# Kernel optimization log

Measured on AMD Instinct MI355X. Metric: run time of the kernel, lower is better.

Reference implementation:

```python
import jax, jax.numpy as jnp
import numpy as np

SIZES = (20, 20, 20, 20, 20)          # formula_oh_sizes
OH_N = sum(SIZES)                      # 100
NUM_BINS = 65536                       # spect_bin.get_num_bins()
EPS_SIZE = 1e-4                        # eps added to subset size
IN_EPS = 1e-5                          # torch InstanceNorm1d default eps


def thermometer_oh(counts):
    # StructuredOneHot with accum=True: per-element thermometer encoding.
    # counts: (N, E) element counts -> (N, sum(SIZES)) with out[j]=1 iff j < count.
    outs = [(jnp.arange(s, dtype=counts.dtype)[None, :] < counts[:, i:i + 1]).astype(jnp.float32)
            for i, s in enumerate(SIZES)]
    return jnp.concatenate(outs, axis=-1)


def inorm(x):
    # InstanceNorm1d (affine=False) as applied here: normalize over last dim per row.
    m = jnp.mean(x, axis=-1, keepdims=True)
    v = jnp.var(x, axis=-1, keepdims=True)
    return (x - m) * jax.lax.rsqrt(v + IN_EPS)


def _lin(key, fan_in, fan_out):
    k1, k2 = jax.random.split(key)
    bound = 1.0 / np.sqrt(fan_in)
    W = jax.random.uniform(k1, (fan_in, fan_out), jnp.float32, -bound, bound)
    b = jax.random.uniform(k2, (fan_out,), jnp.float32, -bound, bound)
    return W, b


def setup_inputs():
    key = jax.random.key(0)
    ks = jax.random.split(key, 12)
    B, A, GF, S, P, E, D = 8, 48, 256, 4096, 32, 5, 256
    vert_feat_in = jax.random.normal(ks[0], (B, A, GF), jnp.float32)
    vert_mask_in = jnp.ones((B, A), jnp.float32)
    elem_idx = jax.random.randint(ks[1], (B, A), 0, E)
    vert_element_oh = jax.nn.one_hot(elem_idx, E, dtype=jnp.float32)
    adj_oh = jnp.zeros((B, A, A), jnp.float32)                      # unused by forward path
    atom_subsets = jax.random.randint(ks[2], (B, S, A), 0, 2).astype(jnp.int32)
    atom_subsets_peaks = jnp.zeros((1,), jnp.float32)               # unused (mass_idx/intensity used)
    mass_idx = jax.random.randint(ks[3], (B, S, P), 0, NUM_BINS).astype(jnp.int32)
    intensity = jax.random.uniform(ks[4], (B, S, P), jnp.float32)
    combine_W, combine_b = _lin(ks[5], OH_N + GF, GF)
    l1_W, l1_b = _lin(ks[6], GF, D)
    l2a_W, l2a_b = _lin(ks[7], D, D)
    l2b_W, l2b_b = _lin(ks[8], D, D)
    score_W, score_b = _lin(ks[9], D, 1)
    return {
        'vert_feat_in': vert_feat_in, 'vert_mask_in': vert_mask_in,
        'vert_element_oh': vert_element_oh, 'adj_oh': adj_oh,
        'atom_subsets': atom_subsets, 'atom_subsets_peaks': atom_subsets_peaks,
        'mass_idx': mass_idx, 'intensity': intensity,
        'combine_W': combine_W, 'combine_b': combine_b,
        'l1_W': l1_W, 'l1_b': l1_b, 'l2a_W': l2a_W, 'l2a_b': l2a_b,
        'l2b_W': l2b_W, 'l2b_b': l2b_b, 'score_W': score_W, 'score_b': score_b,
    }


def reference(vert_feat_in, vert_mask_in, vert_element_oh, adj_oh, atom_subsets,
              atom_subsets_peaks, mass_idx, intensity,
              combine_W, combine_b, l1_W, l1_b, l2a_W, l2a_b, l2b_W, l2b_b,
              score_W, score_b):
    B, A, GF = vert_feat_in.shape
    _, S, _ = atom_subsets.shape
    subsets_f = atom_subsets.astype(jnp.float32)
    masked_vert = vert_feat_in * vert_mask_in[:, :, None]               # (B,A,GF)
    subsets_masked = subsets_f * vert_mask_in[:, None, :]               # (B,S,A)
    # weighted sum of vertex features over each subset
    sws = jnp.einsum('bag,bsa->bsg', masked_vert, subsets_masked)        # (B,S,GF)
    # per-subset element counts -> structured one-hot formula encoding
    counts = jnp.einsum('bae,bsa->bse', vert_element_oh, subsets_f)      # (B,S,E)
    pf_oh = thermometer_oh(counts.reshape(-1, counts.shape[-1])).reshape(B, S, OH_N)
    subset_size = jnp.sum(subsets_masked, axis=2) + EPS_SIZE             # (B,S)
    mean_feat = sws / subset_size[:, :, None]
    normed = inorm(mean_feat)                                            # subset_weighted_norm
    combined = jax.nn.relu(jnp.concatenate([pf_oh, normed], -1) @ combine_W + combine_b)
    x = inorm(combined)                                                  # norm_post_combine
    x = jax.nn.relu(x @ l1_W + l1_b)
    x = jax.nn.leaky_relu(x @ l2a_W + l2a_b)
    x = jax.nn.leaky_relu(x @ l2b_W + l2b_b)
    x = jax.nn.relu(x)
    x = inorm(x)                                                         # norm_pre_score
    scores = (x @ score_W + score_b)[..., 0]                             # (B,S)
    probs = jax.nn.softmax(scores, axis=-1)
    # per-batch sparse mass-matrix binning: scatter-add intensity*prob into spectral bins
    weighted = intensity * probs[:, :, None]                             # (B,S,P)
    seg = jax.vmap(lambda idx, w: jax.ops.segment_sum(w, idx, num_segments=NUM_BINS))
    spect_out = seg(mass_idx.reshape(B, -1), weighted.reshape(B, -1))    # (B,NUM_BINS)
    return spect_out, probs
```

## Files before the change

### kernel.cpp

```cpp
#include <hip/hip_runtime.h>
#include <math.h>

#define B_DIM 8
#define A_DIM 48
#define GF_DIM 256
#define S_DIM 4096
#define P_DIM 32
#define E_DIM 5
#define OHN 100
#define NBINS 65536

typedef __attribute__((ext_vector_type(8))) short short8v;
typedef __attribute__((ext_vector_type(4))) float float4v;

__device__ __forceinline__ float wave_sum(float v) {
#pragma unroll
    for (int o = 32; o; o >>= 1) v += __shfl_xor(v, o, 64);
    return v;
}
__device__ __forceinline__ float wave_max(float v) {
#pragma unroll
    for (int o = 32; o; o >>= 1) v = fmaxf(v, __shfl_xor(v, o, 64));
    return v;
}
__device__ __forceinline__ float quad16_sum(float v) {
    v += __shfl_xor(v, 1, 64); v += __shfl_xor(v, 2, 64);
    v += __shfl_xor(v, 4, 64); v += __shfl_xor(v, 8, 64);
    return v;
}
__device__ __forceinline__ unsigned short bf16_rn(float x) {
    unsigned int u = __float_as_uint(x);
    return (unsigned short)((u + 0x7FFFu + ((u >> 16) & 1u)) >> 16);
}
__device__ __forceinline__ float bf16_val(unsigned short h) {
    return __uint_as_float(((unsigned int)h) << 16);
}
__device__ __forceinline__ float therm_val(int j, float c0, float c1, float c2,
                                           float c3, float c4) {
    int e = j / 20;
    int pos = j - e * 20;
    float ce = (e == 0) ? c0 : (e == 1) ? c1 : (e == 2) ? c2 : (e == 3) ? c3 : c4;
    return ((float)pos < ce) ? 1.0f : 0.0f;
}
__device__ __forceinline__ void g2l16(float* lds, const float* g) {
    __builtin_amdgcn_global_load_lds(
        (const __attribute__((address_space(1))) void*)g,
        (__attribute__((address_space(3))) void*)lds,
        16, 0, 0);
}

__global__ __launch_bounds__(256) void k_wprep(
    const float* __restrict__ cW, const float* __restrict__ l1W,
    const float* __restrict__ l2aW, const float* __restrict__ l2bW,
    short* __restrict__ wp)
{
    int e = blockIdx.x * 256 + threadIdx.x;
    int c = e >> 13;
    int i = e & 8191;
    int nt = i >> 9, lane = (i >> 3) & 63, j = i & 7;
    int krel = (lane >> 4) * 8 + j;
    int n = nt * 16 + (lane & 15);
    float val = 0.f;
    if (c < 12) {
        int kp = c * 32 + krel;
        if (kp < 100)       val = cW[kp * 256 + n];
        else if (kp >= 128) val = cW[(kp - 28) * 256 + n];
    } else {
        int L = (c - 12) >> 3;
        int kc = (c - 12) & 7;
        const float* W = (L == 0) ? l1W : (L == 1) ? l2aW : l2bW;
        val = W[(kc * 32 + krel) * 256 + n];
    }
    unsigned short h = bf16_rn(val);
    float lo = val - bf16_val(h);
    wp[c * 16384 + i]        = (short)h;
    wp[c * 16384 + 8192 + i] = (short)bf16_rn(lo);
}

__global__ __launch_bounds__(256) void k_features(
    const float* __restrict__ vert_feat, const float* __restrict__ vert_mask,
    const float* __restrict__ elem_oh, const int* __restrict__ subsets,
    short* __restrict__ x0h, short* __restrict__ x0l)
{
    __shared__ float4 vertm[A_DIM][GF_DIM / 4];
    __shared__ float  maskL[A_DIM];
    __shared__ int    eiL[A_DIM];

    const int tid  = threadIdx.x;
    const int lane = tid & 63;
    const int w    = tid >> 6;
    const int b    = blockIdx.x >> 9;
    const int s0   = (blockIdx.x & 511) * 8;

    if (tid < A_DIM) {
        maskL[tid] = vert_mask[b * A_DIM + tid];
        int ei = 0;
#pragma unroll
        for (int e = 0; e < E_DIM; ++e)
            if (elem_oh[(b * A_DIM + tid) * E_DIM + e] > 0.5f) ei = e;
        eiL[tid] = ei;
    }
    __syncthreads();

    const float4* vb = (const float4*)(vert_feat + (size_t)b * A_DIM * GF_DIM);
    for (int idx = tid; idx < A_DIM * (GF_DIM / 4); idx += 256) {
        float4 v = vb[idx];
        float mk = maskL[idx >> 6];
        v.x *= mk; v.y *= mk; v.z *= mk; v.w *= mk;
        vertm[idx >> 6][idx & 63] = v;
    }
    __syncthreads();

    const int   myei   = (lane < A_DIM) ? eiL[lane] : -1;
    const float mymask = (lane < A_DIM) ? maskL[lane] : 0.0f;

#pragma unroll
    for (int i = 0; i < 2; ++i) {
        const int s = s0 + w * 2 + i;
        const int* fp = subsets + ((size_t)b * S_DIM + s) * A_DIM;
        int myflag = (lane < A_DIM) ? fp[lane] : 0;
        float fcoef = (float)myflag * mymask;

        float c0, c1, c2, c3, c4;
        {
            unsigned long long m0 = __ballot(myflag != 0 && myei == 0);
            unsigned long long m1 = __ballot(myflag != 0 && myei == 1);
            unsigned long long m2 = __ballot(myflag != 0 && myei == 2);
            unsigned long long m3 = __ballot(myflag != 0 && myei == 3);
            unsigned long long m4 = __ballot(myflag != 0 && myei == 4);
            c0 = (float)__popcll(m0); c1 = (float)__popcll(m1);
            c2 = (float)__popcll(m2); c3 = (float)__popcll(m3);
            c4 = (float)__popcll(m4);
        }
        float ssize = wave_sum(fcoef) + 1e-4f;

        float4 acc = make_float4(0.f, 0.f, 0.f, 0.f);
        for (int a = 0; a < A_DIM; ++a) {
            float cf = __shfl(fcoef, a, 64);
            float4 vv = vertm[a][lane];
            acc.x = fmaf(cf, vv.x, acc.x);
            acc.y = fmaf(cf, vv.y, acc.y);
            acc.z = fmaf(cf, vv.z, acc.z);
            acc.w = fmaf(cf, vv.w, acc.w);
        }
        float inv = 1.0f / ssize;
        float4 mv = make_float4(acc.x * inv, acc.y * inv, acc.z * inv, acc.w * inv);

        float t = wave_sum(mv.x + mv.y + mv.z + mv.w);
        float m = t * (1.0f / 256.0f);
        float dx = mv.x - m, dy = mv.y - m, dz = mv.z - m, dw = mv.w - m;
        float q = wave_sum(dx * dx + dy * dy + dz * dz + dw * dw);
        float rs = 1.0f / sqrtf(q * (1.0f / 256.0f) + 1e-5f);

        const int row = b * S_DIM + s;
        const int fb  = row >> 6;
        const int mloc = row & 63;
        const int mt2 = mloc >> 4;
        const int m15 = mloc & 15;

        {
            int kp = 2 * lane;
            int kc = lane >> 4;
            int qd = (kp & 31) >> 3;
            int j  = kp & 7;
            float t0 = (kp < 100)     ? therm_val(kp, c0, c1, c2, c3, c4) : 0.f;
            float t1 = (kp + 1 < 100) ? therm_val(kp + 1, c0, c1, c2, c3, c4) : 0.f;
            size_t elem = (((size_t)(fb * 12 + kc)) * 4 + mt2) * 512
                        + (qd * 16 + m15) * 8 + j;
            unsigned int wd = (unsigned int)bf16_rn(t0)
                            | ((unsigned int)bf16_rn(t1) << 16);
            ((unsigned int*)x0h)[elem >> 1] = wd;
        }
        {
            float v0 = dx * rs, v1 = dy * rs, v2 = dz * rs, v3 = dw * rs;
            int kc = 4 + (lane >> 3);
            int qd = (lane & 7) >> 1;
            int j  = (lane & 1) * 4;
            size_t eh = (((size_t)(fb * 12 + kc)) * 4 + mt2) * 512
                      + (qd * 16 + m15) * 8 + j;
            unsigned short h0 = bf16_rn(v0), h1 = bf16_rn(v1),
                           h2 = bf16_rn(v2), h3 = bf16_rn(v3);
            uint2 wh; wh.x = (unsigned int)h0 | ((unsigned int)h1 << 16);
            wh.y = (unsigned int)h2 | ((unsigned int)h3 << 16);
            ((uint2*)x0h)[eh >> 2] = wh;
            unsigned short g0 = bf16_rn(v0 - bf16_val(h0)),
                           g1 = bf16_rn(v1 - bf16_val(h1)),
                           g2 = bf16_rn(v2 - bf16_val(h2)),
                           g3 = bf16_rn(v3 - bf16_val(h3));
            size_t el = (((size_t)(fb * 8 + (kc - 4))) * 4 + mt2) * 512
                      + (qd * 16 + m15) * 8 + j;
            uint2 wl; wl.x = (unsigned int)g0 | ((unsigned int)g1 << 16);
            wl.y = (unsigned int)g2 | ((unsigned int)g3 << 16);
            ((uint2*)x0l)[el >> 2] = wl;
        }
    }
}

__device__ __forceinline__ void issue_chunk(short* dst, const short* src, int tid) {
    const float* s = (const float*)src;
    float* d = (float*)dst;
#pragma unroll
    for (int i = 0; i < 4; ++i)
        g2l16(d + i * 2048 + tid * 4, s + i * 2048 + tid * 4);
}

template <int NKC, int LO0, int ACT, bool NORM, bool SCORE>
__device__ __forceinline__ void layer_pass(
    short* xAh, short* xAl, short* wst0, short* wst1, float (*ps)[64],
    const short* __restrict__ wstream, const float* __restrict__ bias,
    const float* __restrict__ sW, const float* __restrict__ sb,
    float* __restrict__ scores, int R0)
{
    const int tid  = threadIdx.x;
    const int lane = tid & 63;
    const int w    = tid >> 6;
    const int wm   = w >> 2;
    const int wn   = w & 3;
    const int quad = lane >> 4;
    const int col  = lane & 15;

    float4v acc[2][4];
#pragma unroll
    for (int mi = 0; mi < 2; ++mi)
#pragma unroll
        for (int nt = 0; nt < 4; ++nt) acc[mi][nt] = (float4v){0.f, 0.f, 0.f, 0.f};

    issue_chunk(wst0, wstream, tid);
    for (int kc = 0; kc < NKC; ++kc) {
        __syncthreads();
        if (kc + 1 < NKC)
            issue_chunk(((kc + 1) & 1) ? wst1 : wst0,
                        wstream + (kc + 1) * 16384, tid);
        const short* wsl = (kc & 1) ? wst1 : wst0;

        short8v ah[2], al[2];
        const bool hlo = (kc >= LO0);
#pragma unroll
        for (int mi = 0; mi < 2; ++mi) {
            ah[mi] = *(const short8v*)(xAh + (((kc) * 4 + wm * 2 + mi) * 64 + lane) * 8);
            if (hlo)
                al[mi] = *(const short8v*)(xAl + (((kc - LO0) * 4 + wm * 2 + mi) * 64 + lane) * 8);
        }
        short8v bh[4], bl[4];
#pragma unroll
        for (int nt = 0; nt < 4; ++nt) {
            bh[nt] = *(const short8v*)(wsl + ((wn * 4 + nt) * 64 + lane) * 8);
            bl[nt] = *(const short8v*)(wsl + 8192 + ((wn * 4 + nt) * 64 + lane) * 8);
        }
#pragma unroll
        for (int mi = 0; mi < 2; ++mi)
#pragma unroll
            for (int nt = 0; nt < 4; ++nt) {
                acc[mi][nt] = __builtin_amdgcn_mfma_f32_16x16x32_bf16(
                    ah[mi], bh[nt], acc[mi][nt], 0, 0, 0);
                acc[mi][nt] = __builtin_amdgcn_mfma_f32_16x16x32_bf16(
                    ah[mi], bl[nt], acc[mi][nt], 0, 0, 0);
                if (hlo)
                    acc[mi][nt] = __builtin_amdgcn_mfma_f32_16x16x32_bf16(
                        al[mi], bh[nt], acc[mi][nt], 0, 0, 0);
            }
    }

    float bcol[4];
#pragma unroll
    for (int nt = 0; nt < 4; ++nt) bcol[nt] = bias[wn * 64 + nt * 16 + col];
#pragma unroll
    for (int mi = 0; mi < 2; ++mi)
#pragma unroll
        for (int nt = 0; nt < 4; ++nt)
#pragma unroll
            for (int r = 0; r < 4; ++r) {
                float z = acc[mi][nt][r] + bcol[nt];
                if (ACT == 0) z = fmaxf(z, 0.f);
                else          z = (z > 0.f) ? z : 0.01f * z;
                acc[mi][nt][r] = z;
            }

    __syncthreads();

    if (NORM) {
        float rsum[2][4];
#pragma unroll
        for (int mi = 0; mi < 2; ++mi)
#pragma unroll
            for (int r = 0; r < 4; ++r)
                rsum[mi][r] = quad16_sum(acc[mi][0][r] + acc[mi][1][r] +
                                         acc[mi][2][r] + acc[mi][3][r]);
        if (col == 0) {
#pragma unroll
            for (int mi = 0; mi < 2; ++mi)
#pragma unroll
                for (int r = 0; r < 4; ++r)
                    ps[wn][wm * 32 + mi * 16 + quad * 4 + r] = rsum[mi][r];
        }
        __syncthreads();
        float mu[2][4];
#pragma unroll
        for (int mi = 0; mi < 2; ++mi)
#pragma unroll
            for (int r = 0; r < 4; ++r) {
                int m = wm * 32 + mi * 16 + quad * 4 + r;
                mu[mi][r] = (ps[0][m] + ps[1][m] + ps[2][m] + ps[3][m]) * (1.f / 256.f);
            }
        __syncthreads();
#pragma unroll
        for (int mi = 0; mi < 2; ++mi)
#pragma unroll
            for (int nt = 0; nt < 4; ++nt)
#pragma unroll
                for (int r = 0; r < 4; ++r) acc[mi][nt][r] -= mu[mi][r];
        float qs[2][4];
#pragma unroll
        for (int mi = 0; mi < 2; ++mi)
#pragma unroll
            for (int r = 0; r < 4; ++r) {
                float q = acc[mi][0][r] * acc[mi][0][r] + acc[mi][1][r] * acc[mi][1][r]
                        + acc[mi][2][r] * acc[mi][2][r] + acc[mi][3][r] * acc[mi][3][r];
                qs[mi][r] = quad16_sum(q);
            }
        if (col == 0) {
#pragma unroll
            for (int mi = 0; mi < 2; ++mi)
#pragma unroll
                for (int r = 0; r < 4; ++r)
                    ps[wn][wm * 32 + mi * 16 + quad * 4 + r] = qs[mi][r];
        }
        __syncthreads();
#pragma unroll
        for (int mi = 0; mi < 2; ++mi)
#pragma unroll
            for (int r = 0; r < 4; ++r) {
                int m = wm * 32 + mi * 16 + quad * 4 + r;
                float vq = (ps[0][m] + ps[1][m] + ps[2][m] + ps[3][m]) * (1.f / 256.f);
                float rs = 1.0f / sqrtf(vq + 1e-5f);
#pragma unroll
                for (int nt = 0; nt < 4; ++nt) acc[mi][nt][r] *= rs;
            }
    }

    if (SCORE) {
        float sv[4];
#pragma unroll
        for (int nt = 0; nt < 4; ++nt) sv[nt] = sW[wn * 64 + nt * 16 + col];
        float psu[2][4];
#pragma unroll
        for (int mi = 0; mi < 2; ++mi)
#pragma unroll
            for (int r = 0; r < 4; ++r) {
                float p = acc[mi][0][r] * sv[0] + acc[mi][1][r] * sv[1]
                        + acc[mi][2][r] * sv[2] + acc[mi][3][r] * sv[3];
                psu[mi][r] = quad16_sum(p);
            }
        __syncthreads();
        if (col == 0) {
#pragma unroll
            for (int mi = 0; mi < 2; ++mi)
#pragma unroll
                for (int r = 0; r < 4; ++r)
                    ps[wn][wm * 32 + mi * 16 + quad * 4 + r] = psu[mi][r];
        }
        __syncthreads();
        if (wn == 0 && col == 0) {
            float sb0 = sb[0];
#pragma unroll
            for (int mi = 0; mi < 2; ++mi)
#pragma unroll
                for (int r = 0; r < 4; ++r) {
                    int m = wm * 32 + mi * 16 + quad * 4 + r;
                    scores[R0 + m] = ps[0][m] + ps[1][m] + ps[2][m] + ps[3][m] + sb0;
                }
        }
    } else {
        const int mt2b = wm * 2;
#pragma unroll
        for (int mi = 0; mi < 2; ++mi) {
#pragma unroll
            for (int nt = 0; nt < 4; ++nt) {
                int n  = wn * 64 + nt * 16 + col;
                int n0 = n & ~1;
                int kc2 = n0 >> 5, q2 = (n0 & 31) >> 3, j0 = n0 & 7;
#pragma unroll
                for (int r = 0; r < 4; ++r) {
                    float v  = acc[mi][nt][r];
                    float pv = __shfl_xor(v, 1, 64);
                    int m15 = quad * 4 + r;
                    int rowidx = (kc2 * 4 + mt2b + mi) * 64 + q2 * 16 + m15;
                    if ((col & 1) == 0) {
                        unsigned int wd = (unsigned int)bf16_rn(v)
                                        | ((unsigned int)bf16_rn(pv) << 16);
                        ((unsigned int*)xAh)[rowidx * 4 + (j0 >> 1)] = wd;
                    } else {
                        float ls = v  - bf16_val(bf16_rn(v));
                        float lp = pv - bf16_val(bf16_rn(pv));
                        unsigned int wd = (unsigned int)bf16_rn(lp)
                                        | ((unsigned int)bf16_rn(ls) << 16);
                        ((unsigned int*)xAl)[rowidx * 4 + (j0 >> 1)] = wd;
                    }
                }
            }
        }
    }
}

__global__ __launch_bounds__(512, 2) void k_mlp_mfma(
    const short* __restrict__ wprep,
    const short* __restrict__ x0h, const short* __restrict__ x0l,
    const float* __restrict__ cb,  const float* __restrict__ l1b,
    const float* __restrict__ l2ab, const float* __restrict__ l2bb,
    const float* __restrict__ sW,  const float* __restrict__ sb,
    float* __restrict__ scores)
{
    __shared__ short xAh[12 * 4 * 64 * 8];
    __shared__ short xAl[8 * 4 * 64 * 8];
    __shared__ short wst[2][16384];
    __shared__ float ps[4][64];

    const int tid = threadIdx.x;
    const int fb  = blockIdx.x;
    const int R0  = fb * 64;

    {
        const float* sh = (const float*)(x0h + (size_t)fb * 24576);
#pragma unroll
        for (int i = 0; i < 6; ++i)
            g2l16((float*)xAh + i * 2048 + tid * 4, sh + i * 2048 + tid * 4);
        const float* sl = (const float*)(x0l + (size_t)fb * 16384);
#pragma unroll
        for (int i = 0; i < 4; ++i)
            g2l16((float*)xAl + i * 2048 + tid * 4, sl + i * 2048 + tid * 4);
    }

    layer_pass<12, 4, 0, true,  false>(xAh, xAl, wst[0], wst[1], ps,
        wprep +  0 * 16384, cb,   nullptr, nullptr, nullptr, R0);
    layer_pass< 8, 0, 0, false, false>(xAh, xAl, wst[0], wst[1], ps,
        wprep + 12 * 16384, l1b,  nullptr, nullptr, nullptr, R0);
    layer_pass< 8, 0, 1, false, false>(xAh, xAl, wst[0], wst[1], ps,
        wprep + 20 * 16384, l2ab, nullptr, nullptr, nullptr, R0);
    layer_pass< 8, 0, 0, true,  true >(xAh, xAl, wst[0], wst[1], ps,
        wprep + 28 * 16384, l2bb, sW, sb, scores, R0);
}

__global__ __launch_bounds__(256) void k_softmax(float* __restrict__ probs) {
    const int b   = blockIdx.x;
    const int tid = threadIdx.x;
    __shared__ float redA[4];
    __shared__ float redB[4];
    float* sp = probs + (size_t)b * S_DIM;

    float v[16];
    float mx = -INFINITY;
#pragma unroll
    for (int i = 0; i < 16; ++i) {
        v[i] = sp[tid + i * 256];
        mx = fmaxf(mx, v[i]);
    }
    mx = wave_max(mx);
    if ((tid & 63) == 0) redA[tid >> 6] = mx;
    __syncthreads();
    mx = fmaxf(fmaxf(redA[0], redA[1]), fmaxf(redA[2], redA[3]));

    float sum = 0.f;
#pragma unroll
    for (int i = 0; i < 16; ++i) {
        v[i] = expf(v[i] - mx);
        sum += v[i];
    }
    sum = wave_sum(sum);
    if ((tid & 63) == 0) redB[tid >> 6] = sum;
    __syncthreads();
    float tot = redB[0] + redB[1] + redB[2] + redB[3];
    float inv = 1.0f / tot;
#pragma unroll
    for (int i = 0; i < 16; ++i) sp[tid + i * 256] = v[i] * inv;
}

__global__ __launch_bounds__(256) void k_zero(float* __restrict__ p, int n) {
    int i = blockIdx.x * 256 + threadIdx.x;
    if (i < n) p[i] = 0.0f;
}

__global__ __launch_bounds__(256) void k_scatter(
    const int*   __restrict__ mass_idx,
    const float* __restrict__ intensity,
    const float* __restrict__ probs,
    float* __restrict__ spect)
{
    int i  = blockIdx.x * 256 + threadIdx.x;
    int bs = i >> 5;
    int b  = i >> 17;
    float w = intensity[i] * probs[bs];
    unsafeAtomicAdd(spect + ((size_t)b << 16) + mass_idx[i], w);
}

extern "C" void kernel_launch(void* const* d_in, const int* in_sizes, int n_in,
                              void* d_out, int out_size, void* d_ws, size_t ws_size,
                              hipStream_t stream) {
    const float* vert_feat = (const float*)d_in[0];
    const float* vert_mask = (const float*)d_in[1];
    const float* elem_oh   = (const float*)d_in[2];
    const int*   subsets   = (const int*)d_in[4];
    const int*   mass_idx  = (const int*)d_in[6];
    const float* intensity = (const float*)d_in[7];
    const float* combine_W = (const float*)d_in[8];
    const float* combine_b = (const float*)d_in[9];
    const float* l1_W      = (const float*)d_in[10];
    const float* l1_b      = (const float*)d_in[11];
    const float* l2a_W     = (const float*)d_in[12];
    const float* l2a_b     = (const float*)d_in[13];
    const float* l2b_W     = (const float*)d_in[14];
    const float* l2b_b     = (const float*)d_in[15];
    const float* score_W   = (const float*)d_in[16];
    const float* score_b   = (const float*)d_in[17];

    float* out   = (float*)d_out;
    float* spect = out;
    float* probs = out + (size_t)B_DIM * NBINS;

    short* wprep = (short*)d_ws;
    short* x0h   = wprep + 36 * 16384;
    short* x0l   = x0h + (size_t)512 * 24576;

    k_wprep<<<1152, 256, 0, stream>>>(combine_W, l1_W, l2a_W, l2b_W, wprep);
    k_features<<<4096, 256, 0, stream>>>(vert_feat, vert_mask, elem_oh, subsets,
                                         x0h, x0l);
    k_mlp_mfma<<<512, 512, 0, stream>>>(wprep, x0h, x0l,
        combine_b, l1_b, l2a_b, l2b_b, score_W, score_b, probs);
    k_softmax<<<B_DIM, 256, 0, stream>>>(probs);
    k_zero<<<(B_DIM * NBINS) / 256, 256, 0, stream>>>(spect, B_DIM * NBINS);
    k_scatter<<<(B_DIM * S_DIM * P_DIM) / 256, 256, 0, stream>>>(
        mass_idx, intensity, probs, spect);
}
```

Before: 295.8 us.

## Fuse feature building into MLP kernel and stream weights directly to registers

```diff
diff --git a/kernel.cpp b/kernel.cpp
--- a/kernel.cpp
+++ b/kernel.cpp
@@ -35,19 +35,6 @@
 __device__ __forceinline__ float bf16_val(unsigned short h) {
     return __uint_as_float(((unsigned int)h) << 16);
 }
-__device__ __forceinline__ float therm_val(int j, float c0, float c1, float c2,
-                                           float c3, float c4) {
-    int e = j / 20;
-    int pos = j - e * 20;
-    float ce = (e == 0) ? c0 : (e == 1) ? c1 : (e == 2) ? c2 : (e == 3) ? c3 : c4;
-    return ((float)pos < ce) ? 1.0f : 0.0f;
-}
-__device__ __forceinline__ void g2l16(float* lds, const float* g) {
-    __builtin_amdgcn_global_load_lds(
-        (const __attribute__((address_space(1))) void*)g,
-        (__attribute__((address_space(3))) void*)lds,
-        16, 0, 0);
-}
 
 __global__ __launch_bounds__(256) void k_wprep(
     const float* __restrict__ cW, const float* __restrict__ l1W,
@@ -57,334 +44,211 @@
     int e = blockIdx.x * 256 + threadIdx.x;
     int c = e >> 13;
     int i = e & 8191;
-    int nt = i >> 9, lane = (i >> 3) & 63, j = i & 7;
+    int j    = i & 7;
+    int lane = (i >> 3) & 63;
+    int nt   = (i >> 9) & 1;
+    int wn   = i >> 10;
     int krel = (lane >> 4) * 8 + j;
-    int n = nt * 16 + (lane & 15);
+    int n    = wn * 32 + nt * 16 + (lane & 15);
     float val = 0.f;
     if (c < 12) {
         int kp = c * 32 + krel;
         if (kp < 100)       val = cW[kp * 256 + n];
         else if (kp >= 128) val = cW[(kp - 28) * 256 + n];
     } else {
-        int L = (c - 12) >> 3;
+        int L  = (c - 12) >> 3;
         int kc = (c - 12) & 7;
         const float* W = (L == 0) ? l1W : (L == 1) ? l2aW : l2bW;
         val = W[(kc * 32 + krel) * 256 + n];
     }
     unsigned short h = bf16_rn(val);
     float lo = val - bf16_val(h);
-    wp[c * 16384 + i]        = (short)h;
-    wp[c * 16384 + 8192 + i] = (short)bf16_rn(lo);
-}
-
-__global__ __launch_bounds__(256) void k_features(
-    const float* __restrict__ vert_feat, const float* __restrict__ vert_mask,
-    const float* __restrict__ elem_oh, const int* __restrict__ subsets,
-    short* __restrict__ x0h, short* __restrict__ x0l)
-{
-    __shared__ float4 vertm[A_DIM][GF_DIM / 4];
-    __shared__ float  maskL[A_DIM];
-    __shared__ int    eiL[A_DIM];
-
-    const int tid  = threadIdx.x;
-    const int lane = tid & 63;
-    const int w    = tid >> 6;
-    const int b    = blockIdx.x >> 9;
-    const int s0   = (blockIdx.x & 511) * 8;
-
-    if (tid < A_DIM) {
-        maskL[tid] = vert_mask[b * A_DIM + tid];
-        int ei = 0;
-#pragma unroll
-        for (int e = 0; e < E_DIM; ++e)
-            if (elem_oh[(b * A_DIM + tid) * E_DIM + e] > 0.5f) ei = e;
-        eiL[tid] = ei;
-    }
-    __syncthreads();
-
-    const float4* vb = (const float4*)(vert_feat + (size_t)b * A_DIM * GF_DIM);
-    for (int idx = tid; idx < A_DIM * (GF_DIM / 4); idx += 256) {
-        float4 v = vb[idx];
-        float mk = maskL[idx >> 6];
-        v.x *= mk; v.y *= mk; v.z *= mk; v.w *= mk;
-        vertm[idx >> 6][idx & 63] = v;
-    }
-    __syncthreads();
-
-    const int   myei   = (lane < A_DIM) ? eiL[lane] : -1;
-    const float mymask = (lane < A_DIM) ? maskL[lane] : 0.0f;
-
-#pragma unroll
-    for (int i = 0; i < 2; ++i) {
-        const int s = s0 + w * 2 + i;
-        const int* fp = subsets + ((size_t)b * S_DIM + s) * A_DIM;
-        int myflag = (lane < A_DIM) ? fp[lane] : 0;
-        float fcoef = (float)myflag * mymask;
-
-        float c0, c1, c2, c3, c4;
-        {
-            unsigned long long m0 = __ballot(myflag != 0 && myei == 0);
-            unsigned long long m1 = __ballot(myflag != 0 && myei == 1);
-            unsigned long long m2 = __ballot(myflag != 0 && myei == 2);
-            unsigned long long m3 = __ballot(myflag != 0 && myei == 3);
-            unsigned long long m4 = __ballot(myflag != 0 && myei == 4);
-            c0 = (float)__popcll(m0); c1 = (float)__popcll(m1);
-            c2 = (float)__popcll(m2); c3 = (float)__popcll(m3);
-            c4 = (float)__popcll(m4);
-        }
-        float ssize = wave_sum(fcoef) + 1e-4f;
-
-        float4 acc = make_float4(0.f, 0.f, 0.f, 0.f);
-        for (int a = 0; a < A_DIM; ++a) {
-            float cf = __shfl(fcoef, a, 64);
-            float4 vv = vertm[a][lane];
-            acc.x = fmaf(cf, vv.x, acc.x);
-            acc.y = fmaf(cf, vv.y, acc.y);
-            acc.z = fmaf(cf, vv.z, acc.z);
-            acc.w = fmaf(cf, vv.w, acc.w);
-        }
-        float inv = 1.0f / ssize;
-        float4 mv = make_float4(acc.x * inv, acc.y * inv, acc.z * inv, acc.w * inv);
-
-        float t = wave_sum(mv.x + mv.y + mv.z + mv.w);
-        float m = t * (1.0f / 256.0f);
-        float dx = mv.x - m, dy = mv.y - m, dz = mv.z - m, dw = mv.w - m;
-        float q = wave_sum(dx * dx + dy * dy + dz * dz + dw * dw);
-        float rs = 1.0f / sqrtf(q * (1.0f / 256.0f) + 1e-5f);
-
-        const int row = b * S_DIM + s;
-        const int fb  = row >> 6;
-        const int mloc = row & 63;
-        const int mt2 = mloc >> 4;
-        const int m15 = mloc & 15;
-
-        {
-            int kp = 2 * lane;
-            int kc = lane >> 4;
-            int qd = (kp & 31) >> 3;
-            int j  = kp & 7;
-            float t0 = (kp < 100)     ? therm_val(kp, c0, c1, c2, c3, c4) : 0.f;
-            float t1 = (kp + 1 < 100) ? therm_val(kp + 1, c0, c1, c2, c3, c4) : 0.f;
-            size_t elem = (((size_t)(fb * 12 + kc)) * 4 + mt2) * 512
-                        + (qd * 16 + m15) * 8 + j;
-            unsigned int wd = (unsigned int)bf16_rn(t0)
-                            | ((unsigned int)bf16_rn(t1) << 16);
-            ((unsigned int*)x0h)[elem >> 1] = wd;
-        }
-        {
-            float v0 = dx * rs, v1 = dy * rs, v2 = dz * rs, v3 = dw * rs;
-            int kc = 4 + (lane >> 3);
-            int qd = (lane & 7) >> 1;
-            int j  = (lane & 1) * 4;
-            size_t eh = (((size_t)(fb * 12 + kc)) * 4 + mt2) * 512
-                      + (qd * 16 + m15) * 8 + j;
-            unsigned short h0 = bf16_rn(v0), h1 = bf16_rn(v1),
-                           h2 = bf16_rn(v2), h3 = bf16_rn(v3);
-            uint2 wh; wh.x = (unsigned int)h0 | ((unsigned int)h1 << 16);
-            wh.y = (unsigned int)h2 | ((unsigned int)h3 << 16);
-            ((uint2*)x0h)[eh >> 2] = wh;
-            unsigned short g0 = bf16_rn(v0 - bf16_val(h0)),
-                           g1 = bf16_rn(v1 - bf16_val(h1)),
-                           g2 = bf16_rn(v2 - bf16_val(h2)),
-                           g3 = bf16_rn(v3 - bf16_val(h3));
-            size_t el = (((size_t)(fb * 8 + (kc - 4))) * 4 + mt2) * 512
-                      + (qd * 16 + m15) * 8 + j;
-            uint2 wl; wl.x = (unsigned int)g0 | ((unsigned int)g1 << 16);
-            wl.y = (unsigned int)g2 | ((unsigned int)g3 << 16);
-            ((uint2*)x0l)[el >> 2] = wl;
-        }
-    }
-}
-
-__device__ __forceinline__ void issue_chunk(short* dst, const short* src, int tid) {
-    const float* s = (const float*)src;
-    float* d = (float*)dst;
-#pragma unroll
-    for (int i = 0; i < 4; ++i)
-        g2l16(d + i * 2048 + tid * 4, s + i * 2048 + tid * 4);
+    int base = c * 16384 + (i & 511);
+    wp[base + (wn * 4 + nt) * 512]     = (short)h;
+    wp[base + (wn * 4 + 2 + nt) * 512] = (short)bf16_rn(lo);
+}
+
+#define OFF_XF   49152
+#define OFF_XAL  115712
+#define OFF_PS   148480
+#define OFF_CNT  150528
+#define OFF_MASK 151808
+#define OFF_EI   152000
+
+__device__ __forceinline__ float4v mfma_bf16(short8v a, short8v b, float4v c) {
+    return __builtin_amdgcn_mfma_f32_16x16x32_bf16(a, b, c, 0, 0, 0);
 }
 
 template <int NKC, int LO0, int ACT, bool NORM, bool SCORE>
 __device__ __forceinline__ void layer_pass(
-    short* xAh, short* xAl, short* wst0, short* wst1, float (*ps)[64],
+    short* xAh, short* xAl, float (*ps)[64],
     const short* __restrict__ wstream, const float* __restrict__ bias,
     const float* __restrict__ sW, const float* __restrict__ sb,
     float* __restrict__ scores, int R0)
 {
     const int tid  = threadIdx.x;
     const int lane = tid & 63;
-    const int w    = tid >> 6;
-    const int wm   = w >> 2;
-    const int wn   = w & 3;
+    const int wn   = tid >> 6;
     const int quad = lane >> 4;
     const int col  = lane & 15;
-
-    float4v acc[2][4];
-#pragma unroll
-    for (int mi = 0; mi < 2; ++mi)
-#pragma unroll
-        for (int nt = 0; nt < 4; ++nt) acc[mi][nt] = (float4v){0.f, 0.f, 0.f, 0.f};
-
-    issue_chunk(wst0, wstream, tid);
+    const short* wbase = wstream + wn * 2048 + lane * 8;
+
+    float4v acc[4][2];
+#pragma unroll
+    for (int mi = 0; mi < 4; ++mi)
+#pragma unroll
+        for (int nt = 0; nt < 2; ++nt) acc[mi][nt] = (float4v){0.f, 0.f, 0.f, 0.f};
+
+    short8v bh[2][2], bl[2][2];
+    bh[0][0] = *(const short8v*)(wbase);
+    bh[0][1] = *(const short8v*)(wbase + 512);
+    bl[0][0] = *(const short8v*)(wbase + 1024);
+    bl[0][1] = *(const short8v*)(wbase + 1536);
+
+#pragma unroll
     for (int kc = 0; kc < NKC; ++kc) {
+        const int cur = kc & 1;
+        if (kc + 1 < NKC) {
+            const short* p = wbase + (kc + 1) * 16384;
+            bh[cur ^ 1][0] = *(const short8v*)(p);
+            bh[cur ^ 1][1] = *(const short8v*)(p + 512);
+            bl[cur ^ 1][0] = *(const short8v*)(p + 1024);
+            bl[cur ^ 1][1] = *(const short8v*)(p + 1536);
+        }
+        short8v ah[4], al[4];
+#pragma unroll
+        for (int mi = 0; mi < 4; ++mi)
+            ah[mi] = *(const short8v*)(xAh + ((kc * 4 + mi) * 64 + lane) * 8);
+        const bool hlo = (kc >= LO0);
+        if (hlo) {
+#pragma unroll
+            for (int mi = 0; mi < 4; ++mi)
+                al[mi] = *(const short8v*)(xAl + (((kc - LO0) * 4 + mi) * 64 + lane) * 8);
+        }
+#pragma unroll
+        for (int mi = 0; mi < 4; ++mi)
+#pragma unroll
+            for (int nt = 0; nt < 2; ++nt) {
+                acc[mi][nt] = mfma_bf16(ah[mi], bh[cur][nt], acc[mi][nt]);
+                acc[mi][nt] = mfma_bf16(ah[mi], bl[cur][nt], acc[mi][nt]);
+                if (hlo)
+                    acc[mi][nt] = mfma_bf16(al[mi], bh[cur][nt], acc[mi][nt]);
+            }
+    }
+
+    float bc0 = bias[wn * 32 + col];
+    float bc1 = bias[wn * 32 + 16 + col];
+#pragma unroll
+    for (int mi = 0; mi < 4; ++mi)
+#pragma unroll
+        for (int r = 0; r < 4; ++r) {
+            float z0 = acc[mi][0][r] + bc0;
+            float z1 = acc[mi][1][r] + bc1;
+            if (ACT == 0) { z0 = fmaxf(z0, 0.f); z1 = fmaxf(z1, 0.f); }
+            else { z0 = (z0 > 0.f) ? z0 : 0.01f * z0; z1 = (z1 > 0.f) ? z1 : 0.01f * z1; }
+            acc[mi][0][r] = z0; acc[mi][1][r] = z1;
+        }
+
+    __syncthreads();
+
+    if (NORM) {
+        float rsum[4][4];
+#pragma unroll
+        for (int mi = 0; mi < 4; ++mi)
+#pragma unroll
+            for (int r = 0; r < 4; ++r)
+                rsum[mi][r] = quad16_sum(acc[mi][0][r] + acc[mi][1][r]);
+        if (col == 0) {
+#pragma unroll
+            for (int mi = 0; mi < 4; ++mi)
+#pragma unroll
+                for (int r = 0; r < 4; ++r)
+                    ps[wn][mi * 16 + quad * 4 + r] = rsum[mi][r];
+        }
         __syncthreads();
-        if (kc + 1 < NKC)
-            issue_chunk(((kc + 1) & 1) ? wst1 : wst0,
-                        wstream + (kc + 1) * 16384, tid);
-        const short* wsl = (kc & 1) ? wst1 : wst0;
-
-        short8v ah[2], al[2];
-        const bool hlo = (kc >= LO0);
-#pragma unroll
-        for (int mi = 0; mi < 2; ++mi) {
-            ah[mi] = *(const short8v*)(xAh + (((kc) * 4 + wm * 2 + mi) * 64 + lane) * 8);
-            if (hlo)
-                al[mi] = *(const short8v*)(xAl + (((kc - LO0) * 4 + wm * 2 + mi) * 64 + lane) * 8);
-        }
-        short8v bh[4], bl[4];
-#pragma unroll
-        for (int nt = 0; nt < 4; ++nt) {
-            bh[nt] = *(const short8v*)(wsl + ((wn * 4 + nt) * 64 + lane) * 8);
-            bl[nt] = *(const short8v*)(wsl + 8192 + ((wn * 4 + nt) * 64 + lane) * 8);
-        }
-#pragma unroll
-        for (int mi = 0; mi < 2; ++mi)
-#pragma unroll
-            for (int nt = 0; nt < 4; ++nt) {
-                acc[mi][nt] = __builtin_amdgcn_mfma_f32_16x16x32_bf16(
-                    ah[mi], bh[nt], acc[mi][nt], 0, 0, 0);
-                acc[mi][nt] = __builtin_amdgcn_mfma_f32_16x16x32_bf16(
-                    ah[mi], bl[nt], acc[mi][nt], 0, 0, 0);
-                if (hlo)
-                    acc[mi][nt] = __builtin_amdgcn_mfma_f32_16x16x32_bf16(
-                        al[mi], bh[nt], acc[mi][nt], 0, 0, 0);
-            }
-    }
-
-    float bcol[4];
-#pragma unroll
-    for (int nt = 0; nt < 4; ++nt) bcol[nt] = bias[wn * 64 + nt * 16 + col];
-#pragma unroll
-    for (int mi = 0; mi < 2; ++mi)
-#pragma unroll
-        for (int nt = 0; nt < 4; ++nt)
+        float mu[4][4];
+#pragma unroll
+        for (int mi = 0; mi < 4; ++mi)
 #pragma unroll
             for (int r = 0; r < 4; ++r) {
-                float z = acc[mi][nt][r] + bcol[nt];
-                if (ACT == 0) z = fmaxf(z, 0.f);
-                else          z = (z > 0.f) ? z : 0.01f * z;
-                acc[mi][nt][r] = z;
-            }
-
-    __syncthreads();
-
-    if (NORM) {
-        float rsum[2][4];
-#pragma unroll
-        for (int mi = 0; mi < 2; ++mi)
+                int m = mi * 16 + quad * 4 + r;
+                float s = 0.f;
+#pragma unroll
+                for (int w = 0; w < 8; ++w) s += ps[w][m];
+                mu[mi][r] = s * (1.f / 256.f);
+            }
+        __syncthreads();
+        float qs[4][4];
+#pragma unroll
+        for (int mi = 0; mi < 4; ++mi)
+#pragma unroll
+            for (int r = 0; r < 4; ++r) {
+                acc[mi][0][r] -= mu[mi][r];
+                acc[mi][1][r] -= mu[mi][r];
+                float q = acc[mi][0][r] * acc[mi][0][r]
+                        + acc[mi][1][r] * acc[mi][1][r];
+                qs[mi][r] = quad16_sum(q);
+            }
+        if (col == 0) {
+#pragma unroll
+            for (int mi = 0; mi < 4; ++mi)
+#pragma unroll
+                for (int r = 0; r < 4; ++r)
+                    ps[wn][mi * 16 + quad * 4 + r] = qs[mi][r];
+        }
+        __syncthreads();
+#pragma unroll
+        for (int mi = 0; mi < 4; ++mi)
+#pragma unroll
+            for (int r = 0; r < 4; ++r) {
+                int m = mi * 16 + quad * 4 + r;
+                float s = 0.f;
+#pragma unroll
+                for (int w = 0; w < 8; ++w) s += ps[w][m];
+                float rsf = 1.0f / sqrtf(s * (1.f / 256.f) + 1e-5f);
+                acc[mi][0][r] *= rsf;
+                acc[mi][1][r] *= rsf;
+            }
+    }
+
+    if (SCORE) {
+        __syncthreads();
+        float sv0 = sW[wn * 32 + col];
+        float sv1 = sW[wn * 32 + 16 + col];
+        float psu[4][4];
+#pragma unroll
+        for (int mi = 0; mi < 4; ++mi)
 #pragma unroll
             for (int r = 0; r < 4; ++r)
-                rsum[mi][r] = quad16_sum(acc[mi][0][r] + acc[mi][1][r] +
-                                         acc[mi][2][r] + acc[mi][3][r]);
+                psu[mi][r] = quad16_sum(acc[mi][0][r] * sv0 + acc[mi][1][r] * sv1);
         if (col == 0) {
 #pragma unroll
-            for (int mi = 0; mi < 2; ++mi)
+            for (int mi = 0; mi < 4; ++mi)
 #pragma unroll
                 for (int r = 0; r < 4; ++r)
-                    ps[wn][wm * 32 + mi * 16 + quad * 4 + r] = rsum[mi][r];
+                    ps[wn][mi * 16 + quad * 4 + r] = psu[mi][r];
         }
         __syncthreads();
-        float mu[2][4];
-#pragma unroll
-        for (int mi = 0; mi < 2; ++mi)
-#pragma unroll
-            for (int r = 0; r < 4; ++r) {
-                int m = wm * 32 + mi * 16 + quad * 4 + r;
-                mu[mi][r] = (ps[0][m] + ps[1][m] + ps[2][m] + ps[3][m]) * (1.f / 256.f);
-            }
-        __syncthreads();
-#pragma unroll
-        for (int mi = 0; mi < 2; ++mi)
-#pragma unroll
-            for (int nt = 0; nt < 4; ++nt)
-#pragma unroll
-                for (int r = 0; r < 4; ++r) acc[mi][nt][r] -= mu[mi][r];
-        float qs[2][4];
-#pragma unroll
-        for (int mi = 0; mi < 2; ++mi)
-#pragma unroll
-            for (int r = 0; r < 4; ++r) {
-                float q = acc[mi][0][r] * acc[mi][0][r] + acc[mi][1][r] * acc[mi][1][r]
-                        + acc[mi][2][r] * acc[mi][2][r] + acc[mi][3][r] * acc[mi][3][r];
-                qs[mi][r] = quad16_sum(q);
-            }
-        if (col == 0) {
-#pragma unroll
-            for (int mi = 0; mi < 2; ++mi)
-#pragma unroll
-                for (int r = 0; r < 4; ++r)
-                    ps[wn][wm * 32 + mi * 16 + quad * 4 + r] = qs[mi][r];
-        }
-        __syncthreads();
-#pragma unroll
-        for (int mi = 0; mi < 2; ++mi)
-#pragma unroll
-            for (int r = 0; r < 4; ++r) {
-                int m = wm * 32 + mi * 16 + quad * 4 + r;
-                float vq = (ps[0][m] + ps[1][m] + ps[2][m] + ps[3][m]) * (1.f / 256.f);
-                float rs = 1.0f / sqrtf(vq + 1e-5f);
-#pragma unroll
-                for (int nt = 0; nt < 4; ++nt) acc[mi][nt][r] *= rs;
-            }
-    }
-
-    if (SCORE) {
-        float sv[4];
-#pragma unroll
-        for (int nt = 0; nt < 4; ++nt) sv[nt] = sW[wn * 64 + nt * 16 + col];
-        float psu[2][4];
-#pragma unroll
-        for (int mi = 0; mi < 2; ++mi)
-#pragma unroll
-            for (int r = 0; r < 4; ++r) {
-                float p = acc[mi][0][r] * sv[0] + acc[mi][1][r] * sv[1]
-                        + acc[mi][2][r] * sv[2] + acc[mi][3][r] * sv[3];
-                psu[mi][r] = quad16_sum(p);
-            }
-        __syncthreads();
-        if (col == 0) {
-#pragma unroll
-            for (int mi = 0; mi < 2; ++mi)
-#pragma unroll
-                for (int r = 0; r < 4; ++r)
-                    ps[wn][wm * 32 + mi * 16 + quad * 4 + r] = psu[mi][r];
-        }
-        __syncthreads();
-        if (wn == 0 && col == 0) {
-            float sb0 = sb[0];
-#pragma unroll
-            for (int mi = 0; mi < 2; ++mi)
-#pragma unroll
-                for (int r = 0; r < 4; ++r) {
-                    int m = wm * 32 + mi * 16 + quad * 4 + r;
-                    scores[R0 + m] = ps[0][m] + ps[1][m] + ps[2][m] + ps[3][m] + sb0;
-                }
+        if (tid < 64) {
+            float s = sb[0];
+#pragma unroll
+            for (int w = 0; w < 8; ++w) s += ps[w][tid];
+            scores[R0 + tid] = s;
         }
     } else {
-        const int mt2b = wm * 2;
-#pragma unroll
-        for (int mi = 0; mi < 2; ++mi) {
-#pragma unroll
-            for (int nt = 0; nt < 4; ++nt) {
-                int n  = wn * 64 + nt * 16 + col;
-                int n0 = n & ~1;
-                int kc2 = n0 >> 5, q2 = (n0 & 31) >> 3, j0 = n0 & 7;
+#pragma unroll
+        for (int mi = 0; mi < 4; ++mi)
+#pragma unroll
+            for (int nt = 0; nt < 2; ++nt) {
+                int nn0 = (wn * 32 + nt * 16 + col) & ~1;
+                int q2  = (nn0 & 31) >> 3;
+                int j0  = nn0 & 7;
 #pragma unroll
                 for (int r = 0; r < 4; ++r) {
                     float v  = acc[mi][nt][r];
                     float pv = __shfl_xor(v, 1, 64);
                     int m15 = quad * 4 + r;
-                    int rowidx = (kc2 * 4 + mt2b + mi) * 64 + q2 * 16 + m15;
+                    int rowidx = (wn * 4 + mi) * 64 + q2 * 16 + m15;
                     if ((col & 1) == 0) {
                         unsigned int wd = (unsigned int)bf16_rn(v)
                                         | ((unsigned int)bf16_rn(pv) << 16);
@@ -398,46 +262,157 @@
                     }
                 }
             }
-        }
-    }
-}
-
-__global__ __launch_bounds__(512, 2) void k_mlp_mfma(
+        __syncthreads();
+    }
+}
+
+__global__ __launch_bounds__(512, 2) void k_mega(
+    const float* __restrict__ vert_feat, const float* __restrict__ vert_mask,
+    const float* __restrict__ elem_oh, const int* __restrict__ subsets,
     const short* __restrict__ wprep,
-    const short* __restrict__ x0h, const short* __restrict__ x0l,
     const float* __restrict__ cb,  const float* __restrict__ l1b,
     const float* __restrict__ l2ab, const float* __restrict__ l2bb,
     const float* __restrict__ sW,  const float* __restrict__ sb,
     float* __restrict__ scores)
 {
-    __shared__ short xAh[12 * 4 * 64 * 8];
-    __shared__ short xAl[8 * 4 * 64 * 8];
-    __shared__ short wst[2][16384];
-    __shared__ float ps[4][64];
-
-    const int tid = threadIdx.x;
-    const int fb  = blockIdx.x;
-    const int R0  = fb * 64;
+    __shared__ __align__(16) char smem[152192];
+    short*  xAh   = (short*)smem;
+    float*  xf    = (float*)(smem + OFF_XF);
+    short*  xAl   = (short*)(smem + OFF_XAL);
+    float (*ps)[64] = (float(*)[64])(smem + OFF_PS);
+    float (*cnt)[5] = (float(*)[5])(smem + OFF_CNT);
+    float*  maskL = (float*)(smem + OFF_MASK);
+    int*    eiL   = (int*)(smem + OFF_EI);
+    float4* vertm = (float4*)smem;
+
+    const int tid  = threadIdx.x;
+    const int lane = tid & 63;
+    const int wn   = tid >> 6;
+    const int fb   = blockIdx.x;
+    const int b    = fb >> 6;
+    const int R0   = fb * 64;
+
+    if (tid < A_DIM) {
+        maskL[tid] = vert_mask[b * A_DIM + tid];
+        int ei = 0;
+#pragma unroll
+        for (int e = 0; e < E_DIM; ++e)
+            if (elem_oh[(b * A_DIM + tid) * E_DIM + e] > 0.5f) ei = e;
+        eiL[tid] = ei;
+    }
+    __syncthreads();
 
     {
-        const float* sh = (const float*)(x0h + (size_t)fb * 24576);
-#pragma unroll
-        for (int i = 0; i < 6; ++i)
-            g2l16((float*)xAh + i * 2048 + tid * 4, sh + i * 2048 + tid * 4);
-        const float* sl = (const float*)(x0l + (size_t)fb * 16384);
-#pragma unroll
-        for (int i = 0; i < 4; ++i)
-            g2l16((float*)xAl + i * 2048 + tid * 4, sl + i * 2048 + tid * 4);
-    }
-
-    layer_pass<12, 4, 0, true,  false>(xAh, xAl, wst[0], wst[1], ps,
-        wprep +  0 * 16384, cb,   nullptr, nullptr, nullptr, R0);
-    layer_pass< 8, 0, 0, false, false>(xAh, xAl, wst[0], wst[1], ps,
-        wprep + 12 * 16384, l1b,  nullptr, nullptr, nullptr, R0);
-    layer_pass< 8, 0, 1, false, false>(xAh, xAl, wst[0], wst[1], ps,
-        wprep + 20 * 16384, l2ab, nullptr, nullptr, nullptr, R0);
-    layer_pass< 8, 0, 0, true,  true >(xAh, xAl, wst[0], wst[1], ps,
-        wprep + 28 * 16384, l2bb, sW, sb, scores, R0);
+        const float4* vb = (const float4*)(vert_feat + (size_t)b * A_DIM * GF_DIM);
+        for (int idx = tid; idx < A_DIM * 64; idx += 512) {
+            float4 v = vb[idx];
+            float mk = maskL[idx >> 6];
+            v.x *= mk; v.y *= mk; v.z *= mk; v.w *= mk;
+            vertm[idx] = v;
+        }
+    }
+    __syncthreads();
+
+    {
+        const float mymask = (lane < A_DIM) ? maskL[lane] : 0.f;
+        const int   myei   = (lane < A_DIM) ? eiL[lane]   : -1;
+#pragma unroll
+        for (int i = 0; i < 8; ++i) {
+            const int r = wn * 8 + i;
+            const int* fp = subsets + ((size_t)fb * 64 + r) * A_DIM;
+            int myflag = (lane < A_DIM) ? fp[lane] : 0;
+            float fcoef = (float)myflag * mymask;
+
+            float c0, c1, c2, c3, c4;
+            {
+                unsigned long long m0 = __ballot(myflag != 0 && myei == 0);
+                unsigned long long m1 = __ballot(myflag != 0 && myei == 1);
+                unsigned long long m2 = __ballot(myflag != 0 && myei == 2);
+                unsigned long long m3 = __ballot(myflag != 0 && myei == 3);
+                unsigned long long m4 = __ballot(myflag != 0 && myei == 4);
+                c0 = (float)__popcll(m0); c1 = (float)__popcll(m1);
+                c2 = (float)__popcll(m2); c3 = (float)__popcll(m3);
+                c4 = (float)__popcll(m4);
+            }
+            float ssize = wave_sum(fcoef) + 1e-4f;
+
+            float4 acc = make_float4(0.f, 0.f, 0.f, 0.f);
+            for (int a = 0; a < A_DIM; ++a) {
+                float cf = __shfl(fcoef, a, 64);
+                float4 vv = vertm[a * 64 + lane];
+                acc.x = fmaf(cf, vv.x, acc.x);
+                acc.y = fmaf(cf, vv.y, acc.y);
+                acc.z = fmaf(cf, vv.z, acc.z);
+                acc.w = fmaf(cf, vv.w, acc.w);
+            }
+            float inv = 1.0f / ssize;
+            float4 mv = make_float4(acc.x * inv, acc.y * inv,
+                                    acc.z * inv, acc.w * inv);
+            float t = wave_sum(mv.x + mv.y + mv.z + mv.w);
+            float m = t * (1.0f / 256.0f);
+            float dx = mv.x - m, dy = mv.y - m, dz = mv.z - m, dw = mv.w - m;
+            float q = wave_sum(dx * dx + dy * dy + dz * dz + dw * dw);
+            float rs = 1.0f / sqrtf(q * (1.0f / 256.0f) + 1e-5f);
+
+            *(float4*)(xf + r * 260 + lane * 4) =
+                make_float4(dx * rs, dy * rs, dz * rs, dw * rs);
+            if (lane == 0) {
+                cnt[r][0] = c0; cnt[r][1] = c1; cnt[r][2] = c2;
+                cnt[r][3] = c3; cnt[r][4] = c4;
+            }
+        }
+    }
+    __syncthreads();
+
+    {
+#pragma unroll
+        for (int g0 = 0; g0 < 6; ++g0) {
+            int g  = tid + g0 * 512;
+            int lt = g & 63;
+            int t2 = g >> 6;
+            int kc = t2 >> 2, mi = t2 & 3;
+            int m  = mi * 16 + (lt & 15);
+            int kb = (lt >> 4) * 8;
+            if (kc < 4) {
+                short8v hv;
+#pragma unroll
+                for (int j = 0; j < 8; ++j) {
+                    int kp = kc * 32 + kb + j;
+                    float val = 0.f;
+                    if (kp < 100) {
+                        int e = kp / 20;
+                        val = ((float)(kp - e * 20) < cnt[m][e]) ? 1.0f : 0.0f;
+                    }
+                    hv[j] = (short)bf16_rn(val);
+                }
+                *(short8v*)(xAh + g * 8) = hv;
+            } else {
+                const float* src = xf + m * 260 + (kc - 4) * 32 + kb;
+                float4 f0 = *(const float4*)(src);
+                float4 f1 = *(const float4*)(src + 4);
+                float fv[8] = {f0.x, f0.y, f0.z, f0.w, f1.x, f1.y, f1.z, f1.w};
+                short8v hv, lv;
+#pragma unroll
+                for (int j = 0; j < 8; ++j) {
+                    unsigned short h = bf16_rn(fv[j]);
+                    hv[j] = (short)h;
+                    lv[j] = (short)bf16_rn(fv[j] - bf16_val(h));
+                }
+                *(short8v*)(xAh + g * 8) = hv;
+                *(short8v*)(xAl + (g - 1024) * 8) = lv;
+            }
+        }
+    }
+    __syncthreads();
+
+    layer_pass<12, 4, 0, true,  false>(xAh, xAl, ps, wprep,
+        cb, nullptr, nullptr, nullptr, R0);
+    layer_pass< 8, 0, 0, false, false>(xAh, xAl, ps, wprep + 12 * 16384,
+        l1b, nullptr, nullptr, nullptr, R0);
+    layer_pass< 8, 0, 1, false, false>(xAh, xAl, ps, wprep + 20 * 16384,
+        l2ab, nullptr, nullptr, nullptr, R0);
+    layer_pass< 8, 0, 0, true,  true >(xAh, xAl, ps, wprep + 28 * 16384,
+        l2bb, sW, sb, scores, R0);
 }
 
 __global__ __launch_bounds__(256) void k_softmax(float* __restrict__ probs) {
@@ -515,16 +490,11 @@
     float* out   = (float*)d_out;
     float* spect = out;
     float* probs = out + (size_t)B_DIM * NBINS;
-
     short* wprep = (short*)d_ws;
-    short* x0h   = wprep + 36 * 16384;
-    short* x0l   = x0h + (size_t)512 * 24576;
 
     k_wprep<<<1152, 256, 0, stream>>>(combine_W, l1_W, l2a_W, l2b_W, wprep);
-    k_features<<<4096, 256, 0, stream>>>(vert_feat, vert_mask, elem_oh, subsets,
-                                         x0h, x0l);
-    k_mlp_mfma<<<512, 512, 0, stream>>>(wprep, x0h, x0l,
-        combine_b, l1_b, l2a_b, l2b_b, score_W, score_b, probs);
+    k_mega<<<512, 512, 0, stream>>>(vert_feat, vert_mask, elem_oh, subsets,
+        wprep, combine_b, l1_b, l2a_b, l2b_b, score_W, score_b, probs);
     k_softmax<<<B_DIM, 256, 0, stream>>>(probs);
     k_zero<<<(B_DIM * NBINS) / 256, 256, 0, stream>>>(spect, B_DIM * NBINS);
     k_scatter<<<(B_DIM * S_DIM * P_DIM) / 256, 256, 0, stream>>>(
```

Measured after the change: 286.1 us. 1.03x faster.
